# Kernel tuning notes

Measured on AMD Instinct MI355X. Metric: run time of the kernel, lower is better.

Reference implementation:

```python
import jax, jax.numpy as jnp
import numpy as np

E = 64      # hidden_dim
FF = 128    # ff_dim
H = 4       # nhead
D = E // H  # head_dim = 16
STEPS = 16  # recursion_steps
IN = 200    # input_dim
B = 131072  # batch


def _ln(h, g, b):
    m = h.mean(-1, keepdims=True)
    v = ((h - m) ** 2).mean(-1, keepdims=True)
    return (h - m) * jax.lax.rsqrt(v + 1e-5) * g + b


def _ffn(h, w1, b1, w2, b2):
    return jax.nn.gelu(h @ w1.T + b1, approximate=False) @ w2.T + b2


def _forward(x, W_in, b_in, g_in, be_in,
             z_in_w, z_in_b, z_out_w, z_out_b,
             z_ffn_w1, z_ffn_b1, z_ffn_w2, z_ffn_b2,
             zn1_g, zn1_b, zn2_g, zn2_b,
             y_in_w, y_in_b, y_out_w, y_out_b,
             y_ffn_w1, y_ffn_b1, y_ffn_w2, y_ffn_b2,
             yn1_g, yn1_b, yn2_g, yn2_b,
             W_out, b_out):
    Bn = x.shape[0]
    x_proj = jax.nn.gelu(_ln(x @ W_in.T + b_in, g_in, be_in), approximate=False)  # [B,E]
    y0 = jnp.zeros((Bn, E), dtype=x.dtype)
    z0 = jnp.zeros((Bn, E), dtype=x.dtype)
    scale = 1.0 / np.sqrt(D).astype(np.float32)
    Wv_y = y_in_w[2 * E:]   # cross-attn over a single kv token: softmax weight == 1,
    bv_y = y_in_b[2 * E:]   # so output = out_proj(v_proj(z)) exactly (no approximation)

    def step(carry, _):
        y, z = carry
        seq = jnp.stack([x_proj, y, z], axis=1)            # [B,3,E]
        qkv = seq @ z_in_w.T + z_in_b                      # [B,3,3E]
        q, k, v = jnp.split(qkv, 3, axis=-1)
        rh = lambda t: t.reshape(Bn, 3, H, D).transpose(0, 2, 1, 3)  # [B,H,3,D]
        q, k, v = rh(q), rh(k), rh(v)
        att = jax.nn.softmax(jnp.einsum('bhsd,bhtd->bhst', q, k) * scale, axis=-1)
        o = jnp.einsum('bhst,bhtd->bhsd', att, v).transpose(0, 2, 1, 3).reshape(Bn, 3, E)
        o = o @ z_out_w.T + z_out_b
        z_res = _ln(z + o[:, 2, :], zn1_g, zn1_b)
        z2 = _ln(z_res + _ffn(z_res, z_ffn_w1, z_ffn_b1, z_ffn_w2, z_ffn_b2), zn2_g, zn2_b)
        ca = (z2 @ Wv_y.T + bv_y) @ y_out_w.T + y_out_b    # 1-token cross-attention
        y_res = _ln(y + ca, yn1_g, yn1_b)
        y2 = _ln(y_res + _ffn(y_res, y_ffn_w1, y_ffn_b1, y_ffn_w2, y_ffn_b2), yn2_g, yn2_b)
        return (y2, z2), None

    (y, z), _ = jax.lax.scan(step, (y0, z0), None, length=STEPS)
    return (y @ W_out.T + b_out)[:, 0]                     # [B]


def setup_inputs() -> dict:
    key = jax.random.key(0)
    ks = jax.random.split(key, 12)
    f = lambda k, s: jax.random.normal(k, s, dtype=jnp.float32) * 0.05
    zeros = lambda s: jnp.zeros(s, dtype=jnp.float32)
    ones = lambda s: jnp.ones(s, dtype=jnp.float32)
    return {
        'x': jax.random.normal(ks[0], (B, IN), dtype=jnp.float32),
        'W_in': f(ks[1], (E, IN)), 'b_in': zeros((E,)),
        'g_in': ones((E,)), 'be_in': zeros((E,)),
        'z_in_w': f(ks[2], (3 * E, E)), 'z_in_b': zeros((3 * E,)),
        'z_out_w': f(ks[3], (E, E)), 'z_out_b': zeros((E,)),
        'z_ffn_w1': f(ks[4], (FF, E)), 'z_ffn_b1': zeros((FF,)),
        'z_ffn_w2': f(ks[5], (E, FF)), 'z_ffn_b2': zeros((E,)),
        'zn1_g': ones((E,)), 'zn1_b': zeros((E,)),
        'zn2_g': ones((E,)), 'zn2_b': zeros((E,)),
        'y_in_w': f(ks[6], (3 * E, E)), 'y_in_b': zeros((3 * E,)),
        'y_out_w': f(ks[7], (E, E)), 'y_out_b': zeros((E,)),
        'y_ffn_w1': f(ks[8], (FF, E)), 'y_ffn_b1': zeros((FF,)),
        'y_ffn_w2': f(ks[9], (E, FF)), 'y_ffn_b2': zeros((E,)),
        'yn1_g': ones((E,)), 'yn1_b': zeros((E,)),
        'yn2_g': ones((E,)), 'yn2_b': zeros((E,)),
        'W_out': f(ks[10], (1, E)), 'b_out': zeros((1,)),
    }


def reference(x, W_in, b_in, g_in, be_in,
              z_in_w, z_in_b, z_out_w, z_out_b,
              z_ffn_w1, z_ffn_b1, z_ffn_w2, z_ffn_b2,
              zn1_g, zn1_b, zn2_g, zn2_b,
              y_in_w, y_in_b, y_out_w, y_out_b,
              y_ffn_w1, y_ffn_b1, y_ffn_w2, y_ffn_b2,
              yn1_g, yn1_b, yn2_g, yn2_b,
              W_out, b_out):
    return _forward(x, W_in, b_in, g_in, be_in,
                    z_in_w, z_in_b, z_out_w, z_out_b,
                    z_ffn_w1, z_ffn_b1, z_ffn_w2, z_ffn_b2,
                    zn1_g, zn1_b, zn2_g, zn2_b,
                    y_in_w, y_in_b, y_out_w, y_out_b,
                    y_ffn_w1, y_ffn_b1, y_ffn_w2, y_ffn_b2,
                    yn1_g, yn1_b, yn2_g, yn2_b,
                    W_out, b_out)
```

## Files before the change

kernel.cpp:

```cpp
#include <hip/hip_runtime.h>
#include <math.h>


constexpr int STEPS = 16;
constexpr int INDIM = 200;

typedef __attribute__((ext_vector_type(8))) short bfrag8;
typedef __attribute__((ext_vector_type(4))) float f32x4;
typedef __attribute__((ext_vector_type(4))) short s16x4;

constexpr int FB_WIN  = 0;
constexpr int NFRAG   = 140;
constexpr int NPARAM  = 1544;

constexpr int LB_ZQ   = 0;
constexpr int LB_ZK   = 8;
constexpr int LB_ZV   = 16;
constexpr int LB_ZOUT = 24;
constexpr int LB_ZF1  = 32;
constexpr int LB_ZF2  = 48;
constexpr int LB_YV   = 64;
constexpr int LB_YOUT = 72;
constexpr int LB_YF1  = 80;
constexpr int LB_YF2  = 96;
constexpr int NSTEADY = 112;

constexpr int PB_BIN   = 0;
constexpr int PB_GIN   = 64;
constexpr int PB_BEIN  = 128;
constexpr int PB_ZINB  = 192;
constexpr int PB_ZOUTB = 384;
constexpr int PB_ZF1B  = 448;
constexpr int PB_ZF2B  = 576;
constexpr int PB_ZN1G  = 640;
constexpr int PB_ZN1B  = 704;
constexpr int PB_ZN2G  = 768;
constexpr int PB_ZN2B  = 832;
constexpr int PB_YVB   = 896;
constexpr int PB_YOUTB = 960;
constexpr int PB_YF1B  = 1024;
constexpr int PB_YF2B  = 1152;
constexpr int PB_YN1G  = 1216;
constexpr int PB_YN1B  = 1280;
constexpr int PB_YN2G  = 1344;
constexpr int PB_YN2B  = 1408;
constexpr int PB_WOUT  = 1472;
constexpr int PB_BOUT  = 1536;

constexpr int S64      = 72;
constexpr int S128     = 136;
constexpr int L_W      = 0;
constexpr int L_P      = 57344;
constexpr int L_ACT    = 60432;
constexpr int WAVE_SH  = 2176;
constexpr int NWAVE    = 8;
constexpr int ARENA_SH = L_ACT + NWAVE * WAVE_SH;

struct Params {
  const float *x, *W_in, *b_in, *g_in, *be_in;
  const float *z_in_w, *z_in_b, *z_out_w, *z_out_b;
  const float *z_ffn_w1, *z_ffn_b1, *z_ffn_w2, *z_ffn_b2;
  const float *zn1_g, *zn1_b, *zn2_g, *zn2_b;
  const float *y_in_w, *y_in_b, *y_out_w, *y_out_b;
  const float *y_ffn_w1, *y_ffn_b1, *y_ffn_w2, *y_ffn_b2;
  const float *yn1_g, *yn1_b, *yn2_g, *yn2_b;
  const float *W_out, *b_out;
  float *out;
  int nrows;
};

__device__ __forceinline__ ushort f2bf(float f) {
  uint u = __float_as_uint(f);
  u += 0x7FFFu + ((u >> 16) & 1u);
  return (ushort)(u >> 16);
}
__device__ __forceinline__ uint pk2(float a, float b) {
  return (uint)f2bf(a) | ((uint)f2bf(b) << 16);
}
__device__ __forceinline__ float upk_lo(uint u) {
  return __uint_as_float(u << 16);
}
__device__ __forceinline__ float upk_hi(uint u) {
  return __uint_as_float(u & 0xFFFF0000u);
}
__device__ __forceinline__ float dot4(f32x4 a, f32x4 b) {
  return a.x * b.x + a.y * b.y + a.z * b.z + a.w * b.w;
}
__device__ __forceinline__ void stc(short* buf, int stride, int mt, int q,
                                    int s, f32x4 c) {
  s16x4 v;
  v.x = (short)f2bf(c.x); v.y = (short)f2bf(c.y);
  v.z = (short)f2bf(c.z); v.w = (short)f2bf(c.w);
  *(s16x4*)(buf + s * stride + mt * 16 + q * 4) = v;
}

__device__ __forceinline__ void c2b_p(const uint p[8], bfrag8& b0, bfrag8& b1,
                                      int lane) {
  const int srcA = (lane & 15) | ((lane & 16) << 1);
  const int srcB = srcA + 16;
  const bool odd = (lane & 32) != 0;
  uint ev0 = p[0], ev1 = p[1], ev2 = p[4], ev3 = p[5];
  uint od0 = p[2], od1 = p[3], od2 = p[6], od3 = p[7];
  uint rA0, rA1, rA2, rA3, rB0, rB1, rB2, rB3;
  {
    uint e, o;
    e = (uint)__shfl((int)ev0, srcA); o = (uint)__shfl((int)od0, srcA); rA0 = odd ? o : e;
    e = (uint)__shfl((int)ev1, srcA); o = (uint)__shfl((int)od1, srcA); rA1 = odd ? o : e;
    e = (uint)__shfl((int)ev2, srcA); o = (uint)__shfl((int)od2, srcA); rA2 = odd ? o : e;
    e = (uint)__shfl((int)ev3, srcA); o = (uint)__shfl((int)od3, srcA); rA3 = odd ? o : e;
    e = (uint)__shfl((int)ev0, srcB); o = (uint)__shfl((int)od0, srcB); rB0 = odd ? o : e;
    e = (uint)__shfl((int)ev1, srcB); o = (uint)__shfl((int)od1, srcB); rB1 = odd ? o : e;
    e = (uint)__shfl((int)ev2, srcB); o = (uint)__shfl((int)od2, srcB); rB2 = odd ? o : e;
    e = (uint)__shfl((int)ev3, srcB); o = (uint)__shfl((int)od3, srcB); rB3 = odd ? o : e;
  }
  union U { uint u[4]; bfrag8 b; };
  U u0, u1;
  u0.u[0] = rA0; u0.u[1] = rA1; u0.u[2] = rB0; u0.u[3] = rB1;
  u1.u[0] = rA2; u1.u[1] = rA3; u1.u[2] = rB2; u1.u[3] = rB3;
  b0 = u0.b; b1 = u1.b;
}
__device__ __forceinline__ void c2b(const f32x4 c[4], bfrag8& b0, bfrag8& b1,
                                    int lane) {
  uint p[8];
#pragma unroll
  for (int mt = 0; mt < 4; ++mt) {
    p[2 * mt]     = pk2(c[mt].x, c[mt].y);
    p[2 * mt + 1] = pk2(c[mt].z, c[mt].w);
  }
  c2b_p(p, b0, b1, lane);
}

template <int MT, int KT>
__device__ __forceinline__ void layerN(const short* in, int stride,
                                       const short* lw, int fbase,
                                       const float* bias, f32x4* c,
                                       int lane, int q, int s) {
  bfrag8 bf[KT];
#pragma unroll
  for (int kt = 0; kt < KT; ++kt)
    bf[kt] = *(const bfrag8*)(in + s * stride + kt * 32 + q * 8);
#pragma unroll
  for (int mt = 0; mt < MT; ++mt)
    c[mt] = *(const f32x4*)(bias + mt * 16 + q * 4);
#pragma unroll
  for (int mt = 0; mt < MT; ++mt) {
#pragma unroll
    for (int kt = 0; kt < KT; ++kt) {
      bfrag8 af = *(const bfrag8*)(lw + (fbase + mt * KT + kt) * 512 + lane * 8);
      c[mt] = __builtin_amdgcn_mfma_f32_16x16x32_bf16(af, bf[kt], c[mt], 0, 0, 0);
    }
  }
}

template <int MT>
__device__ __forceinline__ void layerB(const bfrag8* bf, const short* lw,
                                       int fbase, const float* bias, f32x4* c,
                                       int lane, int q) {
#pragma unroll
  for (int mt = 0; mt < MT; ++mt)
    c[mt] = *(const f32x4*)(bias + mt * 16 + q * 4);
#pragma unroll
  for (int mt = 0; mt < MT; ++mt) {
#pragma unroll
    for (int kt = 0; kt < 2; ++kt) {
      bfrag8 af = *(const bfrag8*)(lw + (fbase + mt * 2 + kt) * 512 + lane * 8);
      c[mt] = __builtin_amdgcn_mfma_f32_16x16x32_bf16(af, bf[kt], c[mt], 0, 0, 0);
    }
  }
}

template <int MT>
__device__ __forceinline__ void layerB2(const bfrag8* bfA, const bfrag8* bfB,
                                        const short* lw, int fbase,
                                        const float* bias, f32x4* cA, f32x4* cB,
                                        int lane, int q) {
#pragma unroll
  for (int mt = 0; mt < MT; ++mt) {
    f32x4 b4 = *(const f32x4*)(bias + mt * 16 + q * 4);
    cA[mt] = b4; cB[mt] = b4;
  }
#pragma unroll
  for (int mt = 0; mt < MT; ++mt) {
#pragma unroll
    for (int kt = 0; kt < 2; ++kt) {
      bfrag8 af = *(const bfrag8*)(lw + (fbase + mt * 2 + kt) * 512 + lane * 8);
      cA[mt] = __builtin_amdgcn_mfma_f32_16x16x32_bf16(af, bfA[kt], cA[mt], 0, 0, 0);
      cB[mt] = __builtin_amdgcn_mfma_f32_16x16x32_bf16(af, bfB[kt], cB[mt], 0, 0, 0);
    }
  }
}

__device__ __forceinline__ void lnorm_c(f32x4 c[4], const float* g,
                                        const float* b, int q) {
  float sm = 0.f;
#pragma unroll
  for (int mt = 0; mt < 4; ++mt) sm += c[mt].x + c[mt].y + c[mt].z + c[mt].w;
  sm += __shfl_xor(sm, 16); sm += __shfl_xor(sm, 32);
  float mean = sm * (1.f / 64.f);
  float vs = 0.f;
#pragma unroll
  for (int mt = 0; mt < 4; ++mt) {
    f32x4 d = c[mt];
    d.x -= mean; d.y -= mean; d.z -= mean; d.w -= mean;
    c[mt] = d;
    vs += d.x * d.x + d.y * d.y + d.z * d.z + d.w * d.w;
  }
  vs += __shfl_xor(vs, 16); vs += __shfl_xor(vs, 32);
  float rs = rsqrtf(vs * (1.f / 64.f) + 1e-5f);
#pragma unroll
  for (int mt = 0; mt < 4; ++mt) {
    f32x4 g4 = *(const f32x4*)(g + mt * 16 + q * 4);
    f32x4 b4 = *(const f32x4*)(b + mt * 16 + q * 4);
    f32x4 v = c[mt];
    v.x = v.x * rs * g4.x + b4.x; v.y = v.y * rs * g4.y + b4.y;
    v.z = v.z * rs * g4.z + b4.z; v.w = v.w * rs * g4.w + b4.w;
    c[mt] = v;
  }
}

__device__ __forceinline__ float gelu1(float x) {
  float ax = fabsf(x) * 0.70710678118654752f;
  float t = __builtin_amdgcn_rcpf(1.0f + 0.3275911f * ax);
  float poly =
      ((((1.061405429f * t - 1.453152027f) * t + 1.421413741f) * t -
        0.284496736f) * t + 0.254829592f) * t;
  float e = __expf(-ax * ax);
  float erfv = copysignf(1.0f - poly * e, x);
  return 0.5f * x * (1.0f + erfv);
}

__global__ void prepack_kernel(Params p, ushort* wf) {
  int f = blockIdx.x;
  int lane = threadIdx.x;

  if (f == NFRAG) {
    float* pw = (float*)(wf + (size_t)NFRAG * 512);
    for (int t = lane; t < NPARAM; t += 64) {
      float v = 0.f;
      if      (t < 64)   v = p.b_in[t];
      else if (t < 128)  v = p.g_in[t - 64];
      else if (t < 192)  v = p.be_in[t - 128];
      else if (t < 384)  v = p.z_in_b[t - 192];
      else if (t < 448)  v = p.z_out_b[t - 384];
      else if (t < 576)  v = p.z_ffn_b1[t - 448];
      else if (t < 640)  v = p.z_ffn_b2[t - 576];
      else if (t < 704)  v = p.zn1_g[t - 640];
      else if (t < 768)  v = p.zn1_b[t - 704];
      else if (t < 832)  v = p.zn2_g[t - 768];
      else if (t < 896)  v = p.zn2_b[t - 832];
      else if (t < 960)  v = p.y_in_b[128 + t - 896];
      else if (t < 1024) v = p.y_out_b[t - 960];
      else if (t < 1152) v = p.y_ffn_b1[t - 1024];
      else if (t < 1216) v = p.y_ffn_b2[t - 1152];
      else if (t < 1280) v = p.yn1_g[t - 1216];
      else if (t < 1344) v = p.yn1_b[t - 1280];
      else if (t < 1408) v = p.yn2_g[t - 1344];
      else if (t < 1472) v = p.yn2_b[t - 1408];
      else if (t < 1536) v = p.W_out[t - 1472];
      else if (t == 1536) v = p.b_out[0];
      pw[t] = v;
    }
    return;
  }

  int q = lane >> 4, r = lane & 15;
  const float* src; int K, mt, kt, l;
  if (f < 28)        { src = p.W_in;                K = 200; mt = f / 7;  kt = f % 7; }
  else if (f < 36)   { l = f - 28;  src = p.z_in_w;            K = 64;  mt = l / 2; kt = l % 2; }
  else if (f < 44)   { l = f - 36;  src = p.z_in_w + 64 * 64;  K = 64;  mt = l / 2; kt = l % 2; }
  else if (f < 52)   { l = f - 44;  src = p.z_in_w + 128 * 64; K = 64;  mt = l / 2; kt = l % 2; }
  else if (f < 60)   { l = f - 52;  src = p.z_out_w;           K = 64;  mt = l / 2; kt = l % 2; }
  else if (f < 76)   { l = f - 60;  src = p.z_ffn_w1;          K = 64;  mt = l / 2; kt = l % 2; }
  else if (f < 92)   { l = f - 76;  src = p.z_ffn_w2;          K = 128; mt = l / 4; kt = l % 4; }
  else if (f < 100)  { l = f - 92;  src = p.y_in_w + 128 * 64; K = 64;  mt = l / 2; kt = l % 2; }
  else if (f < 108)  { l = f - 100; src = p.y_out_w;           K = 64;  mt = l / 2; kt = l % 2; }
  else if (f < 124)  { l = f - 108; src = p.y_ffn_w1;          K = 64;  mt = l / 2; kt = l % 2; }
  else               { l = f - 124; src = p.y_ffn_w2;          K = 128; mt = l / 4; kt = l % 4; }

  int row = mt * 16 + r;
  int col = kt * 32 + q * 8;
  bfrag8 o;
#pragma unroll
  for (int j = 0; j < 8; ++j) {
    int cc = col + j;
    float v = (cc < K) ? src[(size_t)row * K + cc] : 0.0f;
    o[j] = (short)f2bf(v);
  }
  *(bfrag8*)(wf + (size_t)f * 512 + lane * 8) = o;
}

__global__
__attribute__((amdgpu_flat_work_group_size(512, 512), amdgpu_waves_per_eu(2, 2)))
void trm_mfma_kernel(Params p, const ushort* wf) {
  __shared__ __align__(16) short arena[ARENA_SH];
  const int tid = threadIdx.x;
  const int wave = tid >> 6, lane = tid & 63;
  const int q = lane >> 4, s = lane & 15;

  {
    const uint4* srcw = (const uint4*)(wf + (size_t)28 * 512);
    uint4* dstw = (uint4*)(arena + L_W);
    for (int i = tid; i < NSTEADY * 64; i += 512) dstw[i] = srcw[i];
    const uint4* srcp = (const uint4*)(wf + (size_t)NFRAG * 512);
    uint4* dstp = (uint4*)(arena + L_P);
    for (int i = tid; i < NPARAM / 4; i += 512) dstp[i] = srcp[i];
  }
  __syncthreads();

  const short* LW = arena + L_W;
  const float* P  = (const float*)(arena + L_P);
  short* TH = arena + L_ACT + wave * WAVE_SH;

  const int chunks = (p.nrows + 127) / 128;
  for (int ic = blockIdx.x; ic < chunks; ic += gridDim.x) {
    const int row0 = ic * 128 + wave * 16;
    int row = row0 + s;
    if (row >= p.nrows) row = p.nrows - 1;

    bfrag8 xpB[2];
    {
      const float* xr = p.x + (size_t)row * INDIM;
      bfrag8 xb[7];
#pragma unroll
      for (int kt = 0; kt < 7; ++kt) {
        int k0i = kt * 32 + q * 8;
        bfrag8 t;
        if (kt < 6 || q == 0) {
          f32x4 lo = *(const f32x4*)(xr + k0i);
          f32x4 hi = *(const f32x4*)(xr + k0i + 4);
          t[0] = (short)f2bf(lo.x); t[1] = (short)f2bf(lo.y);
          t[2] = (short)f2bf(lo.z); t[3] = (short)f2bf(lo.w);
          t[4] = (short)f2bf(hi.x); t[5] = (short)f2bf(hi.y);
          t[6] = (short)f2bf(hi.z); t[7] = (short)f2bf(hi.w);
        } else {
#pragma unroll
          for (int j = 0; j < 8; ++j) t[j] = 0;
        }
        xb[kt] = t;
      }
      f32x4 c[4];
#pragma unroll
      for (int mt = 0; mt < 4; ++mt)
        c[mt] = *(const f32x4*)(P + PB_BIN + mt * 16 + q * 4);
#pragma unroll
      for (int mt = 0; mt < 4; ++mt)
#pragma unroll
        for (int kt = 0; kt < 7; ++kt) {
          bfrag8 af =
              *(const bfrag8*)(wf + (size_t)(FB_WIN + mt * 7 + kt) * 512 + lane * 8);
          c[mt] = __builtin_amdgcn_mfma_f32_16x16x32_bf16(af, xb[kt], c[mt], 0, 0, 0);
        }
      lnorm_c(c, P + PB_GIN, P + PB_BEIN, q);
#pragma unroll
      for (int mt = 0; mt < 4; ++mt) {
        c[mt].x = gelu1(c[mt].x); c[mt].y = gelu1(c[mt].y);
        c[mt].z = gelu1(c[mt].z); c[mt].w = gelu1(c[mt].w);
      }
      c2b(c, xpB[0], xpB[1], lane);
    }

    uint k0p[8], v0p[8], zCp[8], yCp[8];
    bfrag8 zB[2], yB[2];
    {
      f32x4 ck[4], cv[4];
      layerB<4>(xpB, LW, LB_ZK, P + PB_ZINB + 64, ck, lane, q);
      layerB<4>(xpB, LW, LB_ZV, P + PB_ZINB + 128, cv, lane, q);
#pragma unroll
      for (int mt = 0; mt < 4; ++mt) {
        k0p[2 * mt]     = pk2(ck[mt].x, ck[mt].y);
        k0p[2 * mt + 1] = pk2(ck[mt].z, ck[mt].w);
        v0p[2 * mt]     = pk2(cv[mt].x, cv[mt].y);
        v0p[2 * mt + 1] = pk2(cv[mt].z, cv[mt].w);
        zCp[2 * mt] = 0u; zCp[2 * mt + 1] = 0u;
        yCp[2 * mt] = 0u; yCp[2 * mt + 1] = 0u;
      }
#pragma unroll
      for (int kt = 0; kt < 2; ++kt) {
        bfrag8 t;
#pragma unroll
        for (int j = 0; j < 8; ++j) t[j] = 0;
        zB[kt] = t; yB[kt] = t;
      }
    }

    for (int st = 0; st < STEPS; ++st) {
      float w0[4], w1[4], w2[4], wi[4];
      {
        f32x4 q2[4], kz[4], ky[4];
        layerB<4>(zB, LW, LB_ZQ, P + PB_ZINB, q2, lane, q);
        layerB2<4>(zB, yB, LW, LB_ZK, P + PB_ZINB + 64, kz, ky, lane, q);
#pragma unroll
        for (int mt = 0; mt < 4; ++mt) {
          float a0 = q2[mt].x * upk_lo(k0p[2 * mt]) +
                     q2[mt].y * upk_hi(k0p[2 * mt]) +
                     q2[mt].z * upk_lo(k0p[2 * mt + 1]) +
                     q2[mt].w * upk_hi(k0p[2 * mt + 1]);
          float a1 = dot4(q2[mt], ky[mt]);
          float a2 = dot4(q2[mt], kz[mt]);
          a0 += __shfl_xor(a0, 16); a0 += __shfl_xor(a0, 32);
          a1 += __shfl_xor(a1, 16); a1 += __shfl_xor(a1, 32);
          a2 += __shfl_xor(a2, 16); a2 += __shfl_xor(a2, 32);
          a0 *= 0.25f; a1 *= 0.25f; a2 *= 0.25f;
          float mx = fmaxf(a0, fmaxf(a1, a2));
          float e0 = __expf(a0 - mx), e1 = __expf(a1 - mx), e2 = __expf(a2 - mx);
          w0[mt] = e0; w1[mt] = e1; w2[mt] = e2;
          wi[mt] = __builtin_amdgcn_rcpf(e0 + e1 + e2);
        }
      }
      {
        f32x4 vz[4], vy[4];
        layerB2<4>(zB, yB, LW, LB_ZV, P + PB_ZINB + 128, vz, vy, lane, q);
#pragma unroll
        for (int mt = 0; mt < 4; ++mt) {
          f32x4 o;
          o.x = (upk_lo(v0p[2 * mt])     * w0[mt] + vy[mt].x * w1[mt] +
                 vz[mt].x * w2[mt]) * wi[mt];
          o.y = (upk_hi(v0p[2 * mt])     * w0[mt] + vy[mt].y * w1[mt] +
                 vz[mt].y * w2[mt]) * wi[mt];
          o.z = (upk_lo(v0p[2 * mt + 1]) * w0[mt] + vy[mt].z * w1[mt] +
                 vz[mt].z * w2[mt]) * wi[mt];
          o.w = (upk_hi(v0p[2 * mt + 1]) * w0[mt] + vy[mt].w * w1[mt] +
                 vz[mt].w * w2[mt]) * wi[mt];
          stc(TH, S64, mt, q, s, o);
        }
      }

      uint zrp[8];
      {
        f32x4 zr[4];
        layerN<4, 2>(TH, S64, LW, LB_ZOUT, P + PB_ZOUTB, zr, lane, q, s);
#pragma unroll
        for (int mt = 0; mt < 4; ++mt) {
          zr[mt].x += upk_lo(zCp[2 * mt]);     zr[mt].y += upk_hi(zCp[2 * mt]);
          zr[mt].z += upk_lo(zCp[2 * mt + 1]); zr[mt].w += upk_hi(zCp[2 * mt + 1]);
        }
        lnorm_c(zr, P + PB_ZN1G, P + PB_ZN1B, q);
#pragma unroll
        for (int mt = 0; mt < 4; ++mt) {
          stc(TH, S64, mt, q, s, zr[mt]);
          zrp[2 * mt]     = pk2(zr[mt].x, zr[mt].y);
          zrp[2 * mt + 1] = pk2(zr[mt].z, zr[mt].w);
        }
      }

      f32x4 h8[8];
      layerN<8, 2>(TH, S64, LW, LB_ZF1, P + PB_ZF1B, h8, lane, q, s);
#pragma unroll
      for (int mt = 0; mt < 8; ++mt) {
        h8[mt].x = gelu1(h8[mt].x); h8[mt].y = gelu1(h8[mt].y);
        h8[mt].z = gelu1(h8[mt].z); h8[mt].w = gelu1(h8[mt].w);
        stc(TH, S128, mt, q, s, h8[mt]);
      }
      f32x4 z2[4];
      layerN<4, 4>(TH, S128, LW, LB_ZF2, P + PB_ZF2B, z2, lane, q, s);
#pragma unroll
      for (int mt = 0; mt < 4; ++mt) {
        z2[mt].x += upk_lo(zrp[2 * mt]);     z2[mt].y += upk_hi(zrp[2 * mt]);
        z2[mt].z += upk_lo(zrp[2 * mt + 1]); z2[mt].w += upk_hi(zrp[2 * mt + 1]);
      }
      lnorm_c(z2, P + PB_ZN2G, P + PB_ZN2B, q);
      {
        uint zp[8];
#pragma unroll
        for (int mt = 0; mt < 4; ++mt) {
          zp[2 * mt]     = pk2(z2[mt].x, z2[mt].y);
          zp[2 * mt + 1] = pk2(z2[mt].z, z2[mt].w);
          zCp[2 * mt] = zp[2 * mt]; zCp[2 * mt + 1] = zp[2 * mt + 1];
        }
        c2b_p(zp, zB[0], zB[1], lane);
      }

      f32x4 t4[4];
      layerB<4>(zB, LW, LB_YV, P + PB_YVB, t4, lane, q);
#pragma unroll
      for (int mt = 0; mt < 4; ++mt) stc(TH, S64, mt, q, s, t4[mt]);

      uint yrp[8];
      {
        f32x4 yr[4];
        layerN<4, 2>(TH, S64, LW, LB_YOUT, P + PB_YOUTB, yr, lane, q, s);
#pragma unroll
        for (int mt = 0; mt < 4; ++mt) {
          yr[mt].x += upk_lo(yCp[2 * mt]);     yr[mt].y += upk_hi(yCp[2 * mt]);
          yr[mt].z += upk_lo(yCp[2 * mt + 1]); yr[mt].w += upk_hi(yCp[2 * mt + 1]);
        }
        lnorm_c(yr, P + PB_YN1G, P + PB_YN1B, q);
#pragma unroll
        for (int mt = 0; mt < 4; ++mt) {
          stc(TH, S64, mt, q, s, yr[mt]);
          yrp[2 * mt]     = pk2(yr[mt].x, yr[mt].y);
          yrp[2 * mt + 1] = pk2(yr[mt].z, yr[mt].w);
        }
      }

      layerN<8, 2>(TH, S64, LW, LB_YF1, P + PB_YF1B, h8, lane, q, s);
#pragma unroll
      for (int mt = 0; mt < 8; ++mt) {
        h8[mt].x = gelu1(h8[mt].x); h8[mt].y = gelu1(h8[mt].y);
        h8[mt].z = gelu1(h8[mt].z); h8[mt].w = gelu1(h8[mt].w);
        stc(TH, S128, mt, q, s, h8[mt]);
      }
      f32x4 y2[4];
      layerN<4, 4>(TH, S128, LW, LB_YF2, P + PB_YF2B, y2, lane, q, s);
#pragma unroll
      for (int mt = 0; mt < 4; ++mt) {
        y2[mt].x += upk_lo(yrp[2 * mt]);     y2[mt].y += upk_hi(yrp[2 * mt]);
        y2[mt].z += upk_lo(yrp[2 * mt + 1]); y2[mt].w += upk_hi(yrp[2 * mt + 1]);
      }
      lnorm_c(y2, P + PB_YN2G, P + PB_YN2B, q);
      {
        uint yp[8];
#pragma unroll
        for (int mt = 0; mt < 4; ++mt) {
          yp[2 * mt]     = pk2(y2[mt].x, y2[mt].y);
          yp[2 * mt + 1] = pk2(y2[mt].z, y2[mt].w);
          yCp[2 * mt] = yp[2 * mt]; yCp[2 * mt + 1] = yp[2 * mt + 1];
        }
        c2b_p(yp, yB[0], yB[1], lane);
      }
    }

    float acc = 0.f;
#pragma unroll
    for (int mt = 0; mt < 4; ++mt) {
      f32x4 w4 = *(const f32x4*)(P + PB_WOUT + mt * 16 + q * 4);
      acc += upk_lo(yCp[2 * mt]) * w4.x + upk_hi(yCp[2 * mt]) * w4.y +
             upk_lo(yCp[2 * mt + 1]) * w4.z + upk_hi(yCp[2 * mt + 1]) * w4.w;
    }
    acc += __shfl_xor(acc, 16); acc += __shfl_xor(acc, 32);
    if (q == 0 && (row0 + s) < p.nrows) p.out[row0 + s] = acc + P[PB_BOUT];
  }
}

extern "C" void kernel_launch(void* const* d_in, const int* in_sizes, int n_in,
                              void* d_out, int out_size, void* d_ws,
                              size_t ws_size, hipStream_t stream) {
  Params p;
  const float* const* in = (const float* const*)d_in;
  p.x        = in[0];  p.W_in     = in[1];  p.b_in     = in[2];
  p.g_in     = in[3];  p.be_in    = in[4];
  p.z_in_w   = in[5];  p.z_in_b   = in[6];
  p.z_out_w  = in[7];  p.z_out_b  = in[8];
  p.z_ffn_w1 = in[9];  p.z_ffn_b1 = in[10];
  p.z_ffn_w2 = in[11]; p.z_ffn_b2 = in[12];
  p.zn1_g    = in[13]; p.zn1_b    = in[14];
  p.zn2_g    = in[15]; p.zn2_b    = in[16];
  p.y_in_w   = in[17]; p.y_in_b   = in[18];
  p.y_out_w  = in[19]; p.y_out_b  = in[20];
  p.y_ffn_w1 = in[21]; p.y_ffn_b1 = in[22];
  p.y_ffn_w2 = in[23]; p.y_ffn_b2 = in[24];
  p.yn1_g    = in[25]; p.yn1_b    = in[26];
  p.yn2_g    = in[27]; p.yn2_b    = in[28];
  p.W_out    = in[29]; p.b_out    = in[30];
  p.out      = (float*)d_out;
  p.nrows    = in_sizes[0] / INDIM;

  if (ws_size < (size_t)NFRAG * 1024 + NPARAM * 4) return;
  ushort* wf = (ushort*)d_ws;

  hipLaunchKernelGGL(prepack_kernel, dim3(NFRAG + 1), dim3(64), 0, stream, p, wf);
  hipLaunchKernelGGL(trm_mfma_kernel, dim3(256), dim3(512), 0, stream, p, wf);
}
```

Before: 989.1 us.

## Keep FFN hidden in registers and double waves per block to 16

```diff
diff --git a/kernel.cpp b/kernel.cpp
--- a/kernel.cpp
+++ b/kernel.cpp
@@ -48,12 +48,11 @@
 constexpr int PB_BOUT  = 1536;
 
 constexpr int S64      = 72;
-constexpr int S128     = 136;
 constexpr int L_W      = 0;
 constexpr int L_P      = 57344;
 constexpr int L_ACT    = 60432;
-constexpr int WAVE_SH  = 2176;
-constexpr int NWAVE    = 8;
+constexpr int WAVE_SH  = 1152;
+constexpr int NWAVE    = 16;
 constexpr int ARENA_SH = L_ACT + NWAVE * WAVE_SH;
 
 struct Params {
@@ -130,40 +129,39 @@
   c2b_p(p, b0, b1, lane);
 }
 
-template <int MT, int KT>
-__device__ __forceinline__ void layerN(const short* in, int stride,
-                                       const short* lw, int fbase,
-                                       const float* bias, f32x4* c,
+template <int MT>
+__device__ __forceinline__ void layerN(const short* in, const short* lw,
+                                       int fbase, const float* bias, f32x4* c,
                                        int lane, int q, int s) {
-  bfrag8 bf[KT];
-#pragma unroll
-  for (int kt = 0; kt < KT; ++kt)
-    bf[kt] = *(const bfrag8*)(in + s * stride + kt * 32 + q * 8);
+  bfrag8 bf[2];
+#pragma unroll
+  for (int kt = 0; kt < 2; ++kt)
+    bf[kt] = *(const bfrag8*)(in + s * S64 + kt * 32 + q * 8);
 #pragma unroll
   for (int mt = 0; mt < MT; ++mt)
     c[mt] = *(const f32x4*)(bias + mt * 16 + q * 4);
 #pragma unroll
   for (int mt = 0; mt < MT; ++mt) {
 #pragma unroll
+    for (int kt = 0; kt < 2; ++kt) {
+      bfrag8 af = *(const bfrag8*)(lw + (fbase + mt * 2 + kt) * 512 + lane * 8);
+      c[mt] = __builtin_amdgcn_mfma_f32_16x16x32_bf16(af, bf[kt], c[mt], 0, 0, 0);
+    }
+  }
+}
+
+template <int MT, int KT>
+__device__ __forceinline__ void layerBK(const bfrag8* bf, const short* lw,
+                                        int fbase, const float* bias, f32x4* c,
+                                        int lane, int q) {
+#pragma unroll
+  for (int mt = 0; mt < MT; ++mt)
+    c[mt] = *(const f32x4*)(bias + mt * 16 + q * 4);
+#pragma unroll
+  for (int mt = 0; mt < MT; ++mt) {
+#pragma unroll
     for (int kt = 0; kt < KT; ++kt) {
       bfrag8 af = *(const bfrag8*)(lw + (fbase + mt * KT + kt) * 512 + lane * 8);
-      c[mt] = __builtin_amdgcn_mfma_f32_16x16x32_bf16(af, bf[kt], c[mt], 0, 0, 0);
-    }
-  }
-}
-
-template <int MT>
-__device__ __forceinline__ void layerB(const bfrag8* bf, const short* lw,
-                                       int fbase, const float* bias, f32x4* c,
-                                       int lane, int q) {
-#pragma unroll
-  for (int mt = 0; mt < MT; ++mt)
-    c[mt] = *(const f32x4*)(bias + mt * 16 + q * 4);
-#pragma unroll
-  for (int mt = 0; mt < MT; ++mt) {
-#pragma unroll
-    for (int kt = 0; kt < 2; ++kt) {
-      bfrag8 af = *(const bfrag8*)(lw + (fbase + mt * 2 + kt) * 512 + lane * 8);
       c[mt] = __builtin_amdgcn_mfma_f32_16x16x32_bf16(af, bf[kt], c[mt], 0, 0, 0);
     }
   }
@@ -290,7 +288,7 @@
 }
 
 __global__
-__attribute__((amdgpu_flat_work_group_size(512, 512), amdgpu_waves_per_eu(2, 2)))
+__attribute__((amdgpu_flat_work_group_size(1024, 1024), amdgpu_waves_per_eu(4, 4)))
 void trm_mfma_kernel(Params p, const ushort* wf) {
   __shared__ __align__(16) short arena[ARENA_SH];
   const int tid = threadIdx.x;
@@ -300,10 +298,10 @@
   {
     const uint4* srcw = (const uint4*)(wf + (size_t)28 * 512);
     uint4* dstw = (uint4*)(arena + L_W);
-    for (int i = tid; i < NSTEADY * 64; i += 512) dstw[i] = srcw[i];
+    for (int i = tid; i < NSTEADY * 64; i += 1024) dstw[i] = srcw[i];
     const uint4* srcp = (const uint4*)(wf + (size_t)NFRAG * 512);
     uint4* dstp = (uint4*)(arena + L_P);
-    for (int i = tid; i < NPARAM / 4; i += 512) dstp[i] = srcp[i];
+    for (int i = tid; i < NPARAM / 4; i += 1024) dstp[i] = srcp[i];
   }
   __syncthreads();
 
@@ -311,9 +309,9 @@
   const float* P  = (const float*)(arena + L_P);
   short* TH = arena + L_ACT + wave * WAVE_SH;
 
-  const int chunks = (p.nrows + 127) / 128;
+  const int chunks = (p.nrows + 255) / 256;
   for (int ic = blockIdx.x; ic < chunks; ic += gridDim.x) {
-    const int row0 = ic * 128 + wave * 16;
+    const int row0 = ic * 256 + wave * 16;
     int row = row0 + s;
     if (row >= p.nrows) row = p.nrows - 1;
 
@@ -363,8 +361,8 @@
     bfrag8 zB[2], yB[2];
     {
       f32x4 ck[4], cv[4];
-      layerB<4>(xpB, LW, LB_ZK, P + PB_ZINB + 64, ck, lane, q);
-      layerB<4>(xpB, LW, LB_ZV, P + PB_ZINB + 128, cv, lane, q);
+      layerBK<4, 2>(xpB, LW, LB_ZK, P + PB_ZINB + 64, ck, lane, q);
+      layerBK<4, 2>(xpB, LW, LB_ZV, P + PB_ZINB + 128, cv, lane, q);
 #pragma unroll
       for (int mt = 0; mt < 4; ++mt) {
         k0p[2 * mt]     = pk2(ck[mt].x, ck[mt].y);
@@ -387,7 +385,7 @@
       float w0[4], w1[4], w2[4], wi[4];
       {
         f32x4 q2[4], kz[4], ky[4];
-        layerB<4>(zB, LW, LB_ZQ, P + PB_ZINB, q2, lane, q);
+        layerBK<4, 2>(zB, LW, LB_ZQ, P + PB_ZINB, q2, lane, q);
         layerB2<4>(zB, yB, LW, LB_ZK, P + PB_ZINB + 64, kz, ky, lane, q);
 #pragma unroll
         for (int mt = 0; mt < 4; ++mt) {
@@ -428,7 +426,7 @@
       uint zrp[8];
       {
         f32x4 zr[4];
-        layerN<4, 2>(TH, S64, LW, LB_ZOUT, P + PB_ZOUTB, zr, lane, q, s);
+        layerN<4>(TH, LW, LB_ZOUT, P + PB_ZOUTB, zr, lane, q, s);
 #pragma unroll
         for (int mt = 0; mt < 4; ++mt) {
           zr[mt].x += upk_lo(zCp[2 * mt]);     zr[mt].y += upk_hi(zCp[2 * mt]);
@@ -443,16 +441,26 @@
         }
       }
 
-      f32x4 h8[8];
-      layerN<8, 2>(TH, S64, LW, LB_ZF1, P + PB_ZF1B, h8, lane, q, s);
-#pragma unroll
-      for (int mt = 0; mt < 8; ++mt) {
-        h8[mt].x = gelu1(h8[mt].x); h8[mt].y = gelu1(h8[mt].y);
-        h8[mt].z = gelu1(h8[mt].z); h8[mt].w = gelu1(h8[mt].w);
-        stc(TH, S128, mt, q, s, h8[mt]);
+      bfrag8 hB[4];
+      {
+        f32x4 h8[8];
+        layerN<8>(TH, LW, LB_ZF1, P + PB_ZF1B, h8, lane, q, s);
+#pragma unroll
+        for (int g = 0; g < 2; ++g) {
+          uint ph[8];
+#pragma unroll
+          for (int mt = 0; mt < 4; ++mt) {
+            f32x4 h = h8[4 * g + mt];
+            h.x = gelu1(h.x); h.y = gelu1(h.y);
+            h.z = gelu1(h.z); h.w = gelu1(h.w);
+            ph[2 * mt]     = pk2(h.x, h.y);
+            ph[2 * mt + 1] = pk2(h.z, h.w);
+          }
+          c2b_p(ph, hB[2 * g], hB[2 * g + 1], lane);
+        }
       }
       f32x4 z2[4];
-      layerN<4, 4>(TH, S128, LW, LB_ZF2, P + PB_ZF2B, z2, lane, q, s);
+      layerBK<4, 4>(hB, LW, LB_ZF2, P + PB_ZF2B, z2, lane, q);
 #pragma unroll
       for (int mt = 0; mt < 4; ++mt) {
         z2[mt].x += upk_lo(zrp[2 * mt]);     z2[mt].y += upk_hi(zrp[2 * mt]);
@@ -471,14 +479,14 @@
       }
 
       f32x4 t4[4];
-      layerB<4>(zB, LW, LB_YV, P + PB_YVB, t4, lane, q);
+      layerBK<4, 2>(zB, LW, LB_YV, P + PB_YVB, t4, lane, q);
 #pragma unroll
       for (int mt = 0; mt < 4; ++mt) stc(TH, S64, mt, q, s, t4[mt]);
 
       uint yrp[8];
       {
         f32x4 yr[4];
-        layerN<4, 2>(TH, S64, LW, LB_YOUT, P + PB_YOUTB, yr, lane, q, s);
+        layerN<4>(TH, LW, LB_YOUT, P + PB_YOUTB, yr, lane, q, s);
 #pragma unroll
         for (int mt = 0; mt < 4; ++mt) {
           yr[mt].x += upk_lo(yCp[2 * mt]);     yr[mt].y += upk_hi(yCp[2 * mt]);
@@ -493,15 +501,25 @@
         }
       }
 
-      layerN<8, 2>(TH, S64, LW, LB_YF1, P + PB_YF1B, h8, lane, q, s);
-#pragma unroll
-      for (int mt = 0; mt < 8; ++mt) {
-        h8[mt].x = gelu1(h8[mt].x); h8[mt].y = gelu1(h8[mt].y);
-        h8[mt].z = gelu1(h8[mt].z); h8[mt].w = gelu1(h8[mt].w);
-        stc(TH, S128, mt, q, s, h8[mt]);
+      {
+        f32x4 h8[8];
+        layerN<8>(TH, LW, LB_YF1, P + PB_YF1B, h8, lane, q, s);
+#pragma unroll
+        for (int g = 0; g < 2; ++g) {
+          uint ph[8];
+#pragma unroll
+          for (int mt = 0; mt < 4; ++mt) {
+            f32x4 h = h8[4 * g + mt];
+            h.x = gelu1(h.x); h.y = gelu1(h.y);
+            h.z = gelu1(h.z); h.w = gelu1(h.w);
+            ph[2 * mt]     = pk2(h.x, h.y);
+            ph[2 * mt + 1] = pk2(h.z, h.w);
+          }
+          c2b_p(ph, hB[2 * g], hB[2 * g + 1], lane);
+        }
       }
       f32x4 y2[4];
-      layerN<4, 4>(TH, S128, LW, LB_YF2, P + PB_YF2B, y2, lane, q, s);
+      layerBK<4, 4>(hB, LW, LB_YF2, P + PB_YF2B, y2, lane, q);
 #pragma unroll
       for (int mt = 0; mt < 4; ++mt) {
         y2[mt].x += upk_lo(yrp[2 * mt]);     y2[mt].y += upk_hi(yrp[2 * mt]);
@@ -559,5 +577,5 @@
   ushort* wf = (ushort*)d_ws;
 
   hipLaunchKernelGGL(prepack_kernel, dim3(NFRAG + 1), dim3(64), 0, stream, p, wf);
-  hipLaunchKernelGGL(trm_mfma_kernel, dim3(256), dim3(512), 0, stream, p, wf);
-}
+  hipLaunchKernelGGL(trm_mfma_kernel, dim3(256), dim3(1024), 0, stream, p, wf);
+}
```

New measurement: 974.1 us. No clear change (-1.5%).
